# Kernel tuning notes

Measured on AMD Instinct MI355X. Metric: run time of the kernel, lower is better.

The kernel has to match this reference:

```python
import jax, jax.numpy as jnp
import numpy as np

B = 256; L = 512; PRED = 96; DVARS = 21
P = 16; STRIDE = 16
N = (L - P) // STRIDE + 1      # 32 patches
DM = P * P                     # d_model = 256
K = 5                          # DctAtt low-freq coeffs
EPS_BN = 1e-5


def _dct_mats(n_len):
    # torch_dct DCT-II / DCT-III as dense matrices (exact same scaling as torch_dct)
    n = jnp.arange(n_len, dtype=jnp.float32)
    C = jnp.cos(jnp.pi * (2.0 * n[None, :] + 1.0) * n[:, None] / (2.0 * n_len))  # (k, m)
    D2 = 2.0 * C                                  # dct(x, norm=None):  X = x @ D2.T
    w0 = jnp.where(n == 0, 0.5, 1.0)
    D3 = (C.T * w0[None, :]) / n_len              # idct(X, norm=None): x = X @ D3.T
    rL = jnp.sqrt(jnp.asarray(n_len, jnp.float32))
    s_ortho = jnp.where(n == 0, 0.5 / rL, 0.5 * jnp.sqrt(2.0) / rL)  # unnorm -> ortho scale
    return D2, D3, s_ortho


def _bn(x, g, b):
    # BatchNorm1d, training-mode batch stats (biased var), x: (B, C, Lc)
    m = jnp.mean(x, axis=(0, 2), keepdims=True)
    v = jnp.var(x, axis=(0, 2), keepdims=True)
    return g[None, :, None] * (x - m) * jax.lax.rsqrt(v + EPS_BN) + b[None, :, None]


def _gelu(x):
    return jax.nn.gelu(x, approximate=False)  # torch nn.GELU default = exact erf


def setup_inputs():
    key = jax.random.key(0)
    ks = jax.random.split(key, 24)
    r = lambda i, shp, s=0.02: jax.random.normal(ks[i], shp, jnp.float32) * s
    return dict(
        x=jax.random.normal(ks[0], (B, L, DVARS), jnp.float32),
        w_dct=r(1, (DVARS,), 0.2), b_dct=r(2, (DVARS,), 0.02),
        W_embed=r(3, (P, DM), 0.05), b_embed=r(4, (DM,), 0.02),
        W_linres=r(5, (N * DM, PRED), 0.01), b_linres=r(6, (PRED,), 0.02),
        W_dres=r(7, (DM, P), 0.05), b_dres=r(8, (P,), 0.02),
        w_dc=r(9, (N, P), 0.1), b_dc=r(10, (N,), 0.02),
        w_dc1=r(11, (N, 3), 0.2), b_dc1=r(12, (N,), 0.02),
        g_dctnorm=jnp.ones((DVARS,), jnp.float32), b_dctnorm=jnp.zeros((DVARS,), jnp.float32),
        g_patchnorm=jnp.ones((N,), jnp.float32), b_patchnorm=jnp.zeros((N,), jnp.float32),
        g_depthnorm=jnp.ones((N,), jnp.float32), b_depthnorm=jnp.zeros((N,), jnp.float32),
        thr_p=jnp.array([0.3], jnp.float32),
        W_m1=r(13, (L, PRED), 0.02), b_m1=r(14, (PRED,), 0.02),
        W_m2=r(15, (PRED, PRED), 0.05), b_m2=r(16, (PRED,), 0.02),
        a_dw_w=r(17, (K,), 0.2), a_dw_b=r(18, (), 0.02),
        a_cw=jnp.float32(1.0) + r(19, (), 0.1), a_cb=r(20, (), 0.02),
        a_g=jnp.ones((), jnp.float32), a_b=jnp.zeros((), jnp.float32),
    )


def reference(x, w_dct, b_dct, W_embed, b_embed, W_linres, b_linres,
              W_dres, b_dres, w_dc, b_dc, w_dc1, b_dc1,
              g_dctnorm, b_dctnorm, g_patchnorm, b_patchnorm,
              g_depthnorm, b_depthnorm, thr_p,
              W_m1, b_m1, W_m2, b_m2,
              a_dw_w, a_dw_b, a_cw, a_cb, a_g, a_b):
    Bx = x.shape[0]
    D2, D3, s_ortho = _dct_mats(L)
    xT = jnp.transpose(x, (0, 2, 1))                       # (B,D,L)
    # dctConv = depthwise 1x1 conv => per-channel scale+bias (same layer reused twice)
    x_res = xT * w_dct[:, None] + b_dct[:, None]
    z_dct = xT @ D2.T                                      # dct(norm=None)
    # adaptive_high_freq_mask
    energy = jnp.sum(z_dct * z_dct, axis=-1)               # (B,D)
    med = jnp.median(energy, axis=1, keepdims=True)
    norm_e = energy / (med + 1e-6)
    thr = jnp.quantile(norm_e, thr_p[0])                   # global quantile over all elems
    mask = (norm_e > thr).astype(x.dtype)[..., None]       # broadcasts over freq axis
    z = (z_dct * mask) * w_dct[:, None] + b_dct[:, None]
    z = _gelu(z)
    z = _bn(z, g_dctnorm, b_dctnorm)
    z1 = z @ D3.T + x_res                                  # idct + residual, (B,D,L)
    # patchify (unfold)
    idx = jnp.arange(N)[:, None] * STRIDE + jnp.arange(P)[None, :]
    zp = xT[..., idx].reshape(Bx * DVARS, N, P)            # (BD,N,P)
    z_p = zp @ W_embed + b_embed                           # (BD,N,DM)
    z_res = jnp.transpose(z_p.reshape(Bx, DVARS, N * DM) @ W_linres + b_linres, (0, 2, 1))
    res = z_p @ W_dres + b_dres                            # (BD,N,P)
    # depth_conv: depthwise conv, kernel=P, stride=P over DM=P*P
    zd = jnp.einsum('bnqp,np->bnq', z_p.reshape(Bx * DVARS, N, P, P), w_dc) + b_dc[:, None]
    zd = _bn(zd + res, g_patchnorm, b_patchnorm)
    z2 = _gelu(zd)
    # depth_conv1: depthwise k=3 pad=1
    zpad = jnp.pad(z2, ((0, 0), (0, 0), (1, 1)))
    zc = (w_dc1[:, 0, None] * zpad[..., :-2] + w_dc1[:, 1, None] * zpad[..., 1:-1]
          + w_dc1[:, 2, None] * zpad[..., 2:]) + b_dc1[:, None]
    zc = _bn(zc, g_depthnorm, b_depthnorm)
    zc = _gelu(zc) + z2
    z2f = zc.reshape(Bx, DVARS, N * P)                     # (B,D,L)
    # DctAtt on z1*z2f (low-freq pick + dwConv(k=5,stride=5) + BN(1) + GELU + 1x1 + softmax)
    prod = z1 * z2f
    low = (prod @ D2.T[:, :K]) * s_ortho[:K]               # ortho DCT, first K coeffs (B,D,K)
    att = low @ a_dw_w + a_dw_b                            # (B,D)
    m = jnp.mean(att); v = jnp.var(att)
    att = a_g * (att - m) * jax.lax.rsqrt(v + EPS_BN) + a_b
    att = _gelu(att)
    att1 = jax.nn.softmax(att * a_cw + a_cb, axis=-1)[..., None]  # (B,D,1)
    zsum = z1 * att1 + z2f * (1.0 - att1)
    z_mlp = _gelu(zsum @ W_m1 + b_m1) @ W_m2 + b_m2        # Mlp, (B,D,PRED)
    return z_res + jnp.transpose(z_mlp, (0, 2, 1))         # (B,PRED,D)
```

## Files before the change

kernel.cpp:

```cpp
#include <hip/hip_runtime.h>
#include <hip/hip_bf16.h>

#define B_    256
#define L_    512
#define DV    21
#define NROW  5376
#define NP    32
#define PP    16
#define PRED_ 96

static const size_t OFF_XT    = 0;
static const size_t OFF_ZA    = 2752512;
static const size_t OFF_Z1    = 5505024;
static const size_t OFF_ZCP   = 8257536;
static const size_t OFF_D2    = 11010048;
static const size_t OFF_D3    = 11272192;
static const size_t OFF_TN    = 11583488;
static const size_t OFF_TB    = 11591680;
static const size_t OFF_C     = 11592192;
static const size_t OFF_EN    = 11592320;
static const size_t OFF_NORM  = 11597696;
static const size_t OFF_ATT   = 11603072;
static const size_t OFF_ATT1  = 11608448;
static const size_t OFF_STAT  = 11613824;
static const size_t OFF_ABP   = 11614144;
static const size_t OFF_ABDEP = 11614208;
static const size_t OFF_FLAG  = 11614272;
static const size_t OFF_STG   = 11614336;
static const size_t OFF_T     = 12468816;
static const size_t OFF_PARTP = 15221328;
static const size_t OFF_PARTD = 15307344;
static const size_t OFF_EPART = 15393360;
static const size_t OFF_PARTM = 15436368;
static const size_t OFF_BCAT  = 15447120;
static const size_t OFF_PM    = 15512656;
static const size_t OFF_PC    = 15905872;

static const int S_WDCT=0, S_BDCT=24, S_WE=48, S_BE=4144, S_WL=4400, S_BL=790832,
  S_WD=790928, S_BDRES=795024, S_WDC=795040, S_BDC=795552, S_WDC1=795584, S_BDC1=795680,
  S_GD=795712, S_BDN=795736, S_GP=795760, S_BP=795792, S_GDEP=795824, S_BDEP=795856,
  S_THR=795888, S_WM1=795892, S_BM1=845044, S_WM2=845140, S_BM2=854356,
  S_ADWW=854452, S_ADWB=854460, S_ACW=854464, S_ACB=854468, S_AG=854472, S_AB2=854476;

struct Ptrs { const void* p[30]; };

typedef __attribute__((ext_vector_type(8))) short bf16x8;
typedef __attribute__((ext_vector_type(4))) short bf16x4;
typedef __attribute__((ext_vector_type(4))) float f32x4;

__device__ __forceinline__ float bf2f(unsigned short h){
  unsigned u = ((unsigned)h) << 16;
  return __uint_as_float(u);
}
__device__ __forceinline__ short f2b(float f){
  unsigned u = __float_as_uint(f);
  u = (u + 0x7FFFu + ((u >> 16) & 1u)) >> 16;
  return (short)u;
}
__device__ __forceinline__ float gelu_f(float x){ return 0.5f*x*(1.0f+erff(x*0.70710678118654752440f)); }

#define RD(P,I) (mode ? ((const float*)(P))[(I)] : bf2f(((const unsigned short*)(P))[(I)]))

__global__ __launch_bounds__(256) void k_setup(Ptrs ptrs, float* __restrict__ W,
    float* __restrict__ xt, unsigned short* __restrict__ D2h, unsigned short* __restrict__ D2l,
    unsigned short* __restrict__ D3h, float* __restrict__ dvec,
    float* __restrict__ PM, float* __restrict__ PC,
    float* __restrict__ Tn, float* __restrict__ tb){
  int b = blockIdx.x, tid = threadIdx.x;
  int mode = (((const unsigned*)ptrs.p[13])[0] == 0x3F800000u) ? 1 : 0;
  float* S = W + OFF_STG;
  if (b < 3338){
    const int cnt[29] = {21,21,4096,256,786432,96,4096,16,512,32,96,32,21,21,32,32,32,32,1,49152,96,9216,96,5,1,1,1,1,1};
    const int off[29] = {S_WDCT,S_BDCT,S_WE,S_BE,S_WL,S_BL,S_WD,S_BDRES,S_WDC,S_BDC,S_WDC1,S_BDC1,
                         S_GD,S_BDN,S_GP,S_BP,S_GDEP,S_BDEP,S_THR,S_WM1,S_BM1,S_WM2,S_BM2,
                         S_ADWW,S_ADWB,S_ACW,S_ACB,S_AG,S_AB2};
    int gid = b*256 + tid;
    int a = -1, loc = 0, base = 0;
    #pragma unroll
    for (int i = 0; i < 29; i++){
      if (a < 0 && gid < base + cnt[i]){ a = i; loc = gid - base; }
      base += cnt[i];
    }
    if (a < 0) return;
    S[off[a] + loc] = RD(ptrs.p[a+1], loc);
  } else if (b < 4362){
    __shared__ float xs[128*DV];
    int b2 = b - 3338;
    int bb = b2 >> 2, ch = b2 & 3;
    int l0 = ch*128;
    size_t base = (size_t)bb*(L_*DV) + (size_t)l0*DV;
    for (int i = tid; i < 128*DV; i += 256) xs[i] = RD(ptrs.p[0], base + i);
    __syncthreads();
    for (int i = tid; i < 128*DV; i += 256){
      int d = i >> 7, l = i & 127;
      xt[((size_t)bb*DV + d)*512 + l0 + l] = xs[l*DV + d];
    }
  } else if (b < 5386){
    int i = (b - 4362)*256 + tid;
    int kk = i >> 9, m = i & 511;
    const float PIo = 3.14159265358979323846f / 1024.0f;
    int a = ((2*m+1)*kk) & 2047;
    float v = 2.0f * cosf(PIo * (float)a);
    short hi = f2b(v);
    D2h[i] = (unsigned short)hi;
    D2l[i] = (unsigned short)f2b(v - bf2f((unsigned short)hi));
    int a2 = ((2*kk+1)*m) & 2047;
    float w0 = (m==0) ? 0.5f : 1.0f;
    D3h[i] = (unsigned short)f2b(cosf(PIo * (float)a2) * w0 * (1.0f/512.0f));
    if (i < 512){
      const float rs = 22.627416997969522f;
      float s = 0.f;
      #pragma unroll
      for (int k5 = 0; k5 < 5; k5++){
        float awk = RD(ptrs.p[24], k5);
        float sk = ((k5 == 0) ? 0.5f : 0.70710678118654752440f) / rs;
        int a5 = ((2*i+1)*k5) & 2047;
        s += 2.0f * cosf(PIo * (float)a5) * sk * awk;
      }
      dvec[i] = s;
    }
  } else if (b == 5386){
    W[OFF_STAT + tid] = 0.0f;
    if (tid == 0) *(int*)(W + OFF_FLAG) = mode;
  } else if (b < 6923){
    int bb2 = b - 5387;
    int y = bb2 / 192, xb = bb2 - y*192;
    int gid = xb*256 + tid;
    int l = gid/96, p = gid - l*96;
    int n = l>>4, q = l&15;
    int j0 = y*32;
    float acc = 0.f;
    #pragma unroll 8
    for (int j = j0; j < j0+32; j++)
      acc += RD(ptrs.p[3], q*256+j) * RD(ptrs.p[5], (size_t)(n*256+j)*96 + p);
    PM[(size_t)y*49152 + gid] = acc;
  } else if (b < 7051){
    int blkC = b - 6923;
    int rp = tid >> 7, p = tid & 127;
    if (p >= 96) return;
    float acc = 0.f;
    int J0 = blkC*64;
    for (int j = 0; j < 64; j += 2){
      int J = J0 + j + rp;
      acc += RD(ptrs.p[4], J & 255) * RD(ptrs.p[5], (size_t)J*96 + p);
    }
    if (blkC == 0 && rp == 0) acc += RD(ptrs.p[6], p);
    PC[(blkC*2 + rp)*96 + p] = acc;
  } else {
    __shared__ float WeS[4096];
    __shared__ float WdS[4096];
    __shared__ float wdcS[16];
    __shared__ float beS[256];
    __shared__ float bdresS[16];
    int n = b - 7051;
    for (int i = tid; i < 4096; i += 256){ WeS[i] = RD(ptrs.p[3], i); WdS[i] = RD(ptrs.p[7], i); }
    beS[tid] = RD(ptrs.p[4], tid);
    if (tid < 16){ wdcS[tid] = RD(ptrs.p[9], n*16 + tid); bdresS[tid] = RD(ptrs.p[8], tid); }
    __syncthreads();
    int q2 = tid>>4, q = tid&15;
    float R = 0.f;
    for (int j = 0; j < 256; j++) R += WeS[q2*256+j] * WdS[j*16+q];
    float G = 0.f;
    #pragma unroll
    for (int p = 0; p < 16; p++) G += WeS[q2*256 + q*16 + p] * wdcS[p];
    Tn[n*256 + q2*16 + q] = R + G;
    if (tid < 16){
      float rb = bdresS[tid];
      for (int j = 0; j < 256; j++) rb += beS[j] * WdS[j*16+tid];
      float gb = RD(ptrs.p[10], n);
      #pragma unroll
      for (int p = 0; p < 16; p++) gb += beS[tid*16+p] * wdcS[p];
      tb[n*16+tid] = rb + gb;
    }
  }
}

__global__ __launch_bounds__(256) void k_mega(
    const float* __restrict__ xt, const unsigned short* __restrict__ Bh16,
    const unsigned short* __restrict__ Bl16, float* __restrict__ C,
    float* __restrict__ e_part, const int* __restrict__ flag,
    const float* __restrict__ Tn, const float* __restrict__ tb,
    float* __restrict__ t, float* __restrict__ partP,
    const float* __restrict__ S, const float* __restrict__ PM,
    const float* __restrict__ PC, float* __restrict__ cb, unsigned short* __restrict__ Bt){
  int b = blockIdx.x, tid = threadIdx.x;
  if (b < 672){
    __shared__ short Ahi[64*40];
    __shared__ short Alo[64*40];
    __shared__ short Bhi[64*40];
    __shared__ short Blo[64*40];
    int mode = *flag;
    int bx = b & 7, by = b >> 3;
    int rowBase = by*64, colBase = bx*64;
    int srow = tid>>2, seg = tid&3;
    int r = rowBase + srow;
    int wave = tid>>6, lane = tid&63;
    int m = lane&15, quad = lane>>4;
    f32x4 acc[4] = {};
    for (int k0 = 0; k0 < 512; k0 += 32){
      float4 a0 = *(const float4*)(xt + (size_t)r*512 + k0 + seg*8);
      float4 a1 = *(const float4*)(xt + (size_t)r*512 + k0 + seg*8 + 4);
      bf16x8 ah;
      float av[8] = {a0.x,a0.y,a0.z,a0.w,a1.x,a1.y,a1.z,a1.w};
      #pragma unroll
      for (int j = 0; j < 8; j++) ah[j] = f2b(av[j]);
      *(bf16x8*)(Ahi + srow*40 + seg*8) = ah;
      if (mode){
        bf16x8 al;
        #pragma unroll
        for (int j = 0; j < 8; j++) al[j] = f2b(av[j] - bf2f((unsigned short)ah[j]));
        *(bf16x8*)(Alo + srow*40 + seg*8) = al;
      }
      *(bf16x8*)(Bhi + srow*40 + seg*8) = *(const bf16x8*)(Bh16 + (size_t)(colBase+srow)*512 + k0 + seg*8);
      *(bf16x8*)(Blo + srow*40 + seg*8) = *(const bf16x8*)(Bl16 + (size_t)(colBase+srow)*512 + k0 + seg*8);
      __syncthreads();
      bf16x8 afh = *(bf16x8*)(Ahi + (wave*16 + m)*40 + quad*8);
      #pragma unroll
      for (int tt = 0; tt < 4; tt++){
        bf16x8 bfh = *(bf16x8*)(Bhi + (tt*16 + m)*40 + quad*8);
        bf16x8 bfl = *(bf16x8*)(Blo + (tt*16 + m)*40 + quad*8);
        acc[tt] = __builtin_amdgcn_mfma_f32_16x16x32_bf16(afh, bfh, acc[tt], 0, 0, 0);
        acc[tt] = __builtin_amdgcn_mfma_f32_16x16x32_bf16(afh, bfl, acc[tt], 0, 0, 0);
      }
      if (mode){
        bf16x8 afl = *(bf16x8*)(Alo + (wave*16 + m)*40 + quad*8);
        #pragma unroll
        for (int tt = 0; tt < 4; tt++){
          bf16x8 bfh = *(bf16x8*)(Bhi + (tt*16 + m)*40 + quad*8);
          bf16x8 bfl = *(bf16x8*)(Blo + (tt*16 + m)*40 + quad*8);
          acc[tt] = __builtin_amdgcn_mfma_f32_16x16x32_bf16(afl, bfh, acc[tt], 0, 0, 0);
          acc[tt] = __builtin_amdgcn_mfma_f32_16x16x32_bf16(afl, bfl, acc[tt], 0, 0, 0);
        }
      }
      __syncthreads();
    }
    float es[4] = {};
    #pragma unroll
    for (int tt = 0; tt < 4; tt++){
      #pragma unroll
      for (int i = 0; i < 4; i++){
        int rr = rowBase + wave*16 + quad*4 + i;
        int cc = colBase + tt*16 + m;
        float v = acc[tt][i];
        C[(size_t)rr*512 + cc] = v;
        es[i] += v*v;
      }
    }
    #pragma unroll
    for (int off = 1; off < 16; off <<= 1){
      #pragma unroll
      for (int i = 0; i < 4; i++) es[i] += __shfl_xor(es[i], off);
    }
    if (m == 0){
      #pragma unroll
      for (int i = 0; i < 4; i++){
        int rr = rowBase + wave*16 + quad*4 + i;
        e_part[rr*8 + bx] = es[i];
      }
    }
  } else if (b < 2016){
    int blk = b - 672;
    int n0 = tid >> 4, qq = tid & 15;
    int n1 = n0 + 16;
    float T0[16], T1[16];
    #pragma unroll
    for (int q2 = 0; q2 < 16; q2++){
      T0[q2] = Tn[n0*256 + q2*16 + qq];
      T1[q2] = Tn[n1*256 + q2*16 + qq];
    }
    float tb0 = tb[n0*16 + qq], tb1 = tb[n1*16 + qq];
    float s0 = 0.f, q0 = 0.f, s1 = 0.f, q1 = 0.f;
    #pragma unroll
    for (int rr = 0; rr < 4; rr++){
      int r = blk*4 + rr;
      float x0 = xt[(size_t)r*512 + tid];
      float x1 = xt[(size_t)r*512 + tid + 256];
      float a0 = tb0, a1 = tb1;
      #pragma unroll
      for (int q2 = 0; q2 < 16; q2++){
        a0 += __shfl(x0, q2, 16) * T0[q2];
        a1 += __shfl(x1, q2, 16) * T1[q2];
      }
      t[(size_t)r*512 + tid] = a0;       s0 += a0; q0 += a0*a0;
      t[(size_t)r*512 + tid + 256] = a1; s1 += a1; q1 += a1*a1;
    }
    #pragma unroll
    for (int off = 1; off < 16; off <<= 1){
      s0 += __shfl_xor(s0, off); q0 += __shfl_xor(q0, off);
      s1 += __shfl_xor(s1, off); q1 += __shfl_xor(q1, off);
    }
    if (qq == 0){
      partP[(2*n0)*1344 + blk] = s0; partP[(2*n0+1)*1344 + blk] = q0;
      partP[(2*n1)*1344 + blk] = s1; partP[(2*n1+1)*1344 + blk] = q1;
    }
  } else if (b < 2528){
    int i = (b - 2016)*256 + tid;
    int cc = i >> 9, mm = i & 511;
    float v = 0.f;
    if (cc < 96) v = S[S_WM1 + mm*96 + cc];
    else if (cc >= 128 && cc < 224){
      int idx = mm*96 + (cc - 128);
      #pragma unroll
      for (int y = 0; y < 8; y++) v += PM[(size_t)y*49152 + idx];
    }
    Bt[i] = (unsigned short)f2b(v);
  } else {
    if (tid < 96){
      float a = 0.f;
      for (int j = 0; j < 256; j++) a += PC[j*96 + tid];
      cb[tid] = a;
    }
  }
}

__device__ __forceinline__ void dev_bnfin(const float* part, int P, const float* g,
    const float* bb, float count, float* ab, int c, int tid){
  const float* ps = part + (size_t)(2*c)*P;
  const float* pq = part + (size_t)(2*c+1)*P;
  float s = 0.f, s2 = 0.f;
  for (int i = tid; i < P; i += 256){ s += ps[i]; s2 += pq[i]; }
  for (int off = 32; off; off >>= 1){ s += __shfl_down(s, off); s2 += __shfl_down(s2, off); }
  __shared__ float ws[4][2];
  if ((tid & 63) == 0){ ws[tid>>6][0] = s; ws[tid>>6][1] = s2; }
  __syncthreads();
  if (tid == 0){
    float S1 = ws[0][0]+ws[1][0]+ws[2][0]+ws[3][0];
    float S2 = ws[0][1]+ws[1][1]+ws[2][1]+ws[3][1];
    float mean = S1 / count;
    float var  = S2 / count - mean*mean;
    float al = g[c] * rsqrtf(var + 1e-5f);
    float be = bb[c] - mean * al;
    ab[2*c] = al; ab[2*c+1] = be;
  }
}

__global__ __launch_bounds__(256) void k_mid1(const float* __restrict__ e_part,
    float* __restrict__ en, float* __restrict__ norm,
    const float* __restrict__ partP, const float* __restrict__ S, float* __restrict__ abp){
  int b = blockIdx.x, tid = threadIdx.x;
  if (b == 0){
    for (int r = tid; r < NROW; r += 256){
      float s = 0.f;
      #pragma unroll
      for (int j = 0; j < 8; j++) s += e_part[r*8 + j];
      en[r] = s;
    }
    __syncthreads();
    int bb = tid;
    float v[DV];
    for (int d = 0; d < DV; d++) v[d] = en[bb*DV + d];
    float med = 0.f;
    for (int i = 0; i < DV; i++){
      int rk = 0;
      for (int j = 0; j < DV; j++) rk += (v[j] < v[i]) || (v[j] == v[i] && j < i);
      if (rk == 10) med = v[i];
    }
    float den = med + 1e-6f;
    for (int d = 0; d < DV; d++) norm[bb*DV + d] = v[d] / den;
  } else {
    dev_bnfin(partP, 1344, S + S_GP, S + S_BP, 86016.0f, abp, b - 1, tid);
  }
}

__global__ __launch_bounds__(256) void k_mid2(const float* __restrict__ norm,
    const float* __restrict__ S, float* __restrict__ stat,
    float* __restrict__ t, float* __restrict__ zcp,
    const float* __restrict__ abp, float* __restrict__ partD){
  int b = blockIdx.x, tid = threadIdx.x;
  if (b < 336){
    int cand = tid >> 4, part = tid & 15;
    int idx = b*16 + cand;
    float val = norm[idx];
    int cnt = 0;
    int j0 = part*336;
    for (int j = j0; j < j0 + 336; ++j){
      float v = norm[j];
      cnt += (v < val) || (v == val && j < idx);
    }
    __shared__ int sc[16][17];
    sc[cand][part] = cnt;
    __syncthreads();
    if (part == 0){
      int rank = 0;
      #pragma unroll
      for (int i = 0; i < 16; i++) rank += sc[cand][i];
      float q = S[S_THR];
      float pos = q * 5375.0f;
      int i0 = (int)floorf(pos);
      int i1 = (i0 + 1 > 5375) ? 5375 : i0 + 1;
      if (rank == i0) stat[200] = val;
      if (rank == i1) stat[201] = val;
    }
  } else {
    int blk = b - 336;
    const float* wdc1 = S + S_WDC1;
    const float* bdc1 = S + S_BDC1;
    int n0 = tid >> 4, qq = tid & 15;
    int n1 = n0 + 16;
    float al0 = abp[2*n0], be0 = abp[2*n0+1], al1 = abp[2*n1], be1 = abp[2*n1+1];
    float w00 = wdc1[n0*3], w01 = wdc1[n0*3+1], w02 = wdc1[n0*3+2], bb0 = bdc1[n0];
    float w10 = wdc1[n1*3], w11 = wdc1[n1*3+1], w12 = wdc1[n1*3+2], bb1 = bdc1[n1];
    float s0 = 0.f, q0 = 0.f, s1 = 0.f, q1 = 0.f;
    #pragma unroll
    for (int rr = 0; rr < 4; rr++){
      int r = blk*4 + rr;
      float v0 = t[(size_t)r*512 + tid];
      float v1 = t[(size_t)r*512 + tid + 256];
      float z0  = gelu_f(al0*v0 + be0);
      float z1v = gelu_f(al1*v1 + be1);
      float l0 = __shfl_up(z0, 1, 16);    if (qq == 0)  l0 = 0.f;
      float r0 = __shfl_down(z0, 1, 16);  if (qq == 15) r0 = 0.f;
      float l1 = __shfl_up(z1v, 1, 16);   if (qq == 0)  l1 = 0.f;
      float r1 = __shfl_down(z1v, 1, 16); if (qq == 15) r1 = 0.f;
      float cv0 = w00*l0 + w01*z0  + w02*r0 + bb0;
      float cv1 = w10*l1 + w11*z1v + w12*r1 + bb1;
      zcp[(size_t)r*512 + tid] = cv0;       t[(size_t)r*512 + tid] = z0;
      zcp[(size_t)r*512 + tid + 256] = cv1; t[(size_t)r*512 + tid + 256] = z1v;
      s0 += cv0; q0 += cv0*cv0; s1 += cv1; q1 += cv1*cv1;
    }
    #pragma unroll
    for (int off = 1; off < 16; off <<= 1){
      s0 += __shfl_xor(s0, off); q0 += __shfl_xor(q0, off);
      s1 += __shfl_xor(s1, off); q1 += __shfl_xor(q1, off);
    }
    if (qq == 0){
      partD[(2*n0)*1344 + blk] = s0; partD[(2*n0+1)*1344 + blk] = q0;
      partD[(2*n1)*1344 + blk] = s1; partD[(2*n1+1)*1344 + blk] = q1;
    }
  }
}

__global__ __launch_bounds__(256) void k_mid3(float* __restrict__ zA, const float* __restrict__ norm,
    const float* __restrict__ stat, const float* __restrict__ S,
    float* __restrict__ partM, const float* __restrict__ partD, float* __restrict__ abdep){
  int b = blockIdx.x, tid = threadIdx.x;
  if (b < NROW){
    int r = b;
    int d = r % DV, brow = r / DV;
    float q = S[S_THR];
    float pos = q * 5375.0f; float f = pos - floorf(pos);
    float thr = stat[200] + (stat[201] - stat[200]) * f;
    float mask = norm[r] > thr ? 1.0f : 0.0f;
    float w = S[S_WDCT + d], bb = S[S_BDCT + d];
    float s = 0.f, s2 = 0.f;
    for (int i = tid; i < 512; i += 256){
      float v = zA[(size_t)r*512 + i] * mask * w + bb;
      float g = gelu_f(v);
      zA[(size_t)r*512 + i] = g;
      s += g; s2 += g*g;
    }
    for (int off = 32; off; off >>= 1){ s += __shfl_down(s, off); s2 += __shfl_down(s2, off); }
    __shared__ float wsum[4][2];
    int wv = tid >> 6;
    if ((tid & 63) == 0){ wsum[wv][0] = s; wsum[wv][1] = s2; }
    __syncthreads();
    if (tid == 0){
      float SS  = wsum[0][0]+wsum[1][0]+wsum[2][0]+wsum[3][0];
      float SS2 = wsum[0][1]+wsum[1][1]+wsum[2][1]+wsum[3][1];
      partM[(2*d)*256 + brow] = SS;
      partM[(2*d+1)*256 + brow] = SS2;
    }
  } else {
    dev_bnfin(partD, 1344, S + S_GDEP, S + S_BDEP, 86016.0f, abdep, b - NROW, tid);
  }
}

__global__ __launch_bounds__(256) void k_gemm1(
    const float* __restrict__ A, const unsigned short* __restrict__ Bg,
    float* __restrict__ C, const float* __restrict__ partM, const float* __restrict__ xt,
    const float* __restrict__ S){
  __shared__ short Ah[64*40];
  __shared__ short Bh[64*40];
  __shared__ float redS[84];
  __shared__ float abdS[42];
  int tid = threadIdx.x;
  if (tid < 84){
    int s = tid >> 1, h = tid & 1;
    const float* ps = partM + (size_t)s*256 + h*128;
    float a = 0.f;
    #pragma unroll 16
    for (int i = 0; i < 128; i++) a += ps[i];
    redS[tid] = a;
  }
  __syncthreads();
  if (tid < DV){
    float S1 = redS[(2*tid)*2] + redS[(2*tid)*2+1];
    float S2 = redS[(2*tid+1)*2] + redS[(2*tid+1)*2+1];
    float mean = S1 / 131072.0f;
    float var  = S2 / 131072.0f - mean*mean;
    float al = S[S_GD + tid] * rsqrtf(var + 1e-5f);
    abdS[2*tid] = al;
    abdS[2*tid+1] = S[S_BDN + tid] - mean * al;
  }
  __syncthreads();
  int rowBase = blockIdx.y*64, colBase = blockIdx.x*64;
  int srow = tid>>2, seg = tid&3;
  int r = rowBase + srow;
  int d0 = r % DV;
  float alpha = abdS[2*d0], beta = abdS[2*d0+1];
  int wave = tid>>6, lane = tid&63;
  int m = lane&15, quad = lane>>4;
  f32x4 acc[4] = {};
  for (int k0 = 0; k0 < 512; k0 += 32){
    float4 a0 = *(const float4*)(A + (size_t)r*512 + k0 + seg*8);
    float4 a1 = *(const float4*)(A + (size_t)r*512 + k0 + seg*8 + 4);
    a0.x = alpha*a0.x+beta; a0.y = alpha*a0.y+beta; a0.z = alpha*a0.z+beta; a0.w = alpha*a0.w+beta;
    a1.x = alpha*a1.x+beta; a1.y = alpha*a1.y+beta; a1.z = alpha*a1.z+beta; a1.w = alpha*a1.w+beta;
    bf16x8 av;
    av[0]=f2b(a0.x); av[1]=f2b(a0.y); av[2]=f2b(a0.z); av[3]=f2b(a0.w);
    av[4]=f2b(a1.x); av[5]=f2b(a1.y); av[6]=f2b(a1.z); av[7]=f2b(a1.w);
    *(bf16x8*)(Ah + srow*40 + seg*8) = av;
    bf16x8 bv = *(const bf16x8*)(Bg + (size_t)(colBase+srow)*512 + k0 + seg*8);
    *(bf16x8*)(Bh + srow*40 + seg*8) = bv;
    __syncthreads();
    bf16x8 af = *(bf16x8*)(Ah + (wave*16 + m)*40 + quad*8);
    #pragma unroll
    for (int t = 0; t < 4; t++){
      bf16x8 bf = *(bf16x8*)(Bh + (t*16 + m)*40 + quad*8);
      acc[t] = __builtin_amdgcn_mfma_f32_16x16x32_bf16(af, bf, acc[t], 0, 0, 0);
    }
    __syncthreads();
  }
  #pragma unroll
  for (int t = 0; t < 4; t++){
    #pragma unroll
    for (int i = 0; i < 4; i++){
      int rr = rowBase + wave*16 + quad*4 + i;
      int cc = colBase + t*16 + m;
      int d = rr % DV;
      float v = acc[t][i] + xt[(size_t)rr*512 + cc]*S[S_WDCT + d] + S[S_BDCT + d];
      C[(size_t)rr*512 + cc] = v;
    }
  }
}

__global__ __launch_bounds__(256) void k_z2fatt(float* __restrict__ zcp, const float* __restrict__ z2,
    const float* __restrict__ ab, const float* __restrict__ z1,
    const float* __restrict__ dvec, float* __restrict__ att){
  int r = blockIdx.x, tid = threadIdx.x;
  size_t base = (size_t)r*512;
  float s = 0.f;
  #pragma unroll
  for (int h = 0; h < 2; h++){
    int idx = tid + h*256;
    int n = (idx >> 4) & 31;
    float v = gelu_f(ab[2*n]*zcp[base+idx] + ab[2*n+1]) + z2[base+idx];
    zcp[base+idx] = v;
    s += z1[base+idx] * v * dvec[idx];
  }
  for (int off = 32; off; off >>= 1) s += __shfl_down(s, off);
  __shared__ float ws[4];
  if ((tid & 63) == 0) ws[tid>>6] = s;
  __syncthreads();
  if (tid == 0) att[r] = ws[0]+ws[1]+ws[2]+ws[3];
}

__global__ __launch_bounds__(256) void k_gemm_out(
    const float* __restrict__ z1, const float* __restrict__ zcp, const float* __restrict__ xt,
    const unsigned short* __restrict__ Bg, const float* __restrict__ att,
    const float* __restrict__ cb, const float* __restrict__ S,
    void* __restrict__ outv, const int* __restrict__ flag){
  __shared__ short Amix[16*40];
  __shared__ short Axt[16*40];
  __shared__ short Bst[256*40];
  __shared__ float Hs[16*260];
  __shared__ float att1S[16];
  __shared__ float asum[2];
  __shared__ float ws[4][2];
  int bb = blockIdx.x, tid = threadIdx.x;
  int r0 = bb*16;
  {
    float s = 0.f, s2 = 0.f;
    for (int i = tid; i < NROW; i += 256){ float a = att[i]; s += a; s2 += a*a; }
    for (int off = 32; off; off >>= 1){ s += __shfl_down(s, off); s2 += __shfl_down(s2, off); }
    if ((tid & 63) == 0){ ws[tid>>6][0] = s; ws[tid>>6][1] = s2; }
    __syncthreads();
    if (tid == 0){
      asum[0] = ws[0][0]+ws[1][0]+ws[2][0]+ws[3][0];
      asum[1] = ws[0][1]+ws[1][1]+ws[2][1]+ws[3][1];
    }
    __syncthreads();
  }
  if (tid < 16){
    int r = r0 + tid; int b2 = r / DV, d = r - b2*DV;
    float mean = asum[0] / 5376.0f;
    float var  = asum[1] / 5376.0f - mean*mean;
    float al = S[S_AG] * rsqrtf(var + 1e-5f);
    float bbx = S[S_AB2];
    float cw = S[S_ACW], cb2 = S[S_ACB];
    float v[DV]; float mx = -1e30f;
    for (int dd = 0; dd < DV; dd++){
      float a = att[b2*DV + dd];
      a = gelu_f(al*(a - mean) + bbx);
      a = a*cw + cb2;
      v[dd] = a; mx = fmaxf(mx, a);
    }
    float ss = 0.f;
    for (int dd = 0; dd < DV; dd++) ss += expf(v[dd] - mx);
    att1S[tid] = expf(v[d] - mx) / ss;
  }
  __syncthreads();
  int wave = tid>>6, lane = tid&63;
  int m = lane&15, quad = lane>>4;
  f32x4 acc[4] = {};
  for (int k0 = 0; k0 < 512; k0 += 32){
    if (tid < 128){
      int srow = tid >> 3, seg = tid & 7;
      int r = r0 + srow;
      float a1r = att1S[srow];
      float4 zf = *(const float4*)(z1  + (size_t)r*512 + k0 + seg*4);
      float4 cf = *(const float4*)(zcp + (size_t)r*512 + k0 + seg*4);
      float om = 1.0f - a1r;
      bf16x4 mv;
      mv[0] = f2b(a1r*zf.x + om*cf.x); mv[1] = f2b(a1r*zf.y + om*cf.y);
      mv[2] = f2b(a1r*zf.z + om*cf.z); mv[3] = f2b(a1r*zf.w + om*cf.w);
      *(bf16x4*)(Amix + srow*40 + seg*4) = mv;
      float4 xf = *(const float4*)(xt + (size_t)r*512 + k0 + seg*4);
      bf16x4 xv;
      xv[0] = f2b(xf.x); xv[1] = f2b(xf.y); xv[2] = f2b(xf.z); xv[3] = f2b(xf.w);
      *(bf16x4*)(Axt + srow*40 + seg*4) = xv;
    }
    #pragma unroll
    for (int cg = 0; cg < 4; cg++){
      int col = cg*64 + (tid>>2);
      *(bf16x8*)(Bst + col*40 + (tid&3)*8) = *(const bf16x8*)(Bg + (size_t)col*512 + k0 + (tid&3)*8);
    }
    __syncthreads();
    const short* Ast = (wave < 2) ? Amix : Axt;
    bf16x8 af = *(bf16x8*)(Ast + m*40 + quad*8);
    #pragma unroll
    for (int tc = 0; tc < 4; tc++){
      bf16x8 bf = *(bf16x8*)(Bst + (wave*64 + tc*16 + m)*40 + quad*8);
      acc[tc] = __builtin_amdgcn_mfma_f32_16x16x32_bf16(af, bf, acc[tc], 0, 0, 0);
    }
    __syncthreads();
  }
  #pragma unroll
  for (int tc = 0; tc < 4; tc++){
    #pragma unroll
    for (int i = 0; i < 4; i++){
      int col = wave*64 + tc*16 + m;
      Hs[(quad*4 + i)*260 + col] = acc[tc][i];
    }
  }
  __syncthreads();
  for (int i = tid; i < 16*96; i += 256){
    int rr = i / 96, k = i - rr*96;
    Hs[rr*260 + k] = gelu_f(Hs[rr*260 + k] + S[S_BM1 + k]);
  }
  __syncthreads();
  int rr = tid >> 4, pg = tid & 15;
  const float* W2g = S + S_WM2;
  float accv[6] = {};
  for (int k = 0; k < 96; k++){
    float h = Hs[rr*260 + k];
    #pragma unroll
    for (int j = 0; j < 6; j++) accv[j] += h * W2g[k*96 + pg*6 + j];
  }
  int rg = r0 + rr;
  int b2 = rg / DV, d = rg - b2*DV;
  int mode = *flag;
  #pragma unroll
  for (int j = 0; j < 6; j++){
    int p = pg*6 + j;
    float val = Hs[rr*260 + 128 + p] + cb[p] + accv[j] + S[S_BM2 + p];
    size_t oi = ((size_t)b2*96 + p)*DV + d;
    if (mode) ((float*)outv)[oi] = val;
    else ((__hip_bfloat16*)outv)[oi] = __float2bfloat16(val);
  }
}

extern "C" void kernel_launch(void* const* d_in, const int* in_sizes, int n_in,
                              void* d_out, int out_size, void* d_ws, size_t ws_size,
                              hipStream_t stream) {
  float* w = (float*)d_ws;
  float* xt   = w + OFF_XT;
  float* zA   = w + OFF_ZA;
  float* z1   = w + OFF_Z1;
  float* zcp  = w + OFF_ZCP;
  unsigned short* D2h = (unsigned short*)(w + OFF_D2);
  unsigned short* D2l = (unsigned short*)(w + OFF_D2 + 131072);
  unsigned short* D3h = (unsigned short*)(w + OFF_D3);
  float* Tn   = w + OFF_TN;
  float* tb   = w + OFF_TB;
  float* cb   = w + OFF_C;
  float* en   = w + OFF_EN;
  float* nrm  = w + OFF_NORM;
  float* att  = w + OFF_ATT;
  float* dvec = w + OFF_ATT1;
  float* stat = w + OFF_STAT;
  float* abp  = w + OFF_ABP;
  float* abdep= w + OFF_ABDEP;
  int*   flag = (int*)(w + OFF_FLAG);
  float* S    = w + OFF_STG;
  float* tbuf = w + OFF_T;
  float* partP = w + OFF_PARTP;
  float* partD = w + OFF_PARTD;
  float* e_part= w + OFF_EPART;
  float* partM = w + OFF_PARTM;
  unsigned short* BcatTh = (unsigned short*)(w + OFF_BCAT);
  float* PM   = w + OFF_PM;
  float* PC   = w + OFF_PC;

  Ptrs ptrs;
  for (int i = 0; i < 30; i++) ptrs.p[i] = d_in[i];

  k_setup<<<7083, 256, 0, stream>>>(ptrs, w, xt, D2h, D2l, D3h, dvec, PM, PC, Tn, tb);
  k_mega<<<2529, 256, 0, stream>>>(xt, D2h, D2l, zA, e_part, flag, Tn, tb, tbuf, partP, S, PM, PC, cb, BcatTh);
  k_mid1<<<33, 256, 0, stream>>>(e_part, en, nrm, partP, S, abp);
  k_mid2<<<1680, 256, 0, stream>>>(nrm, S, stat, tbuf, zcp, abp, partD);
  k_mid3<<<NROW + NP, 256, 0, stream>>>(zA, nrm, stat, S, partM, partD, abdep);
  k_gemm1<<<dim3(8,84), 256, 0, stream>>>(zA, D3h, z1, partM, xt, S);
  k_z2fatt<<<NROW, 256, 0, stream>>>(zcp, tbuf, abdep, z1, dvec, att);
  k_gemm_out<<<336, 256, 0, stream>>>(z1, zcp, xt, BcatTh, att, cb, S, d_out, flag);
}
```

Before: 291.0 us.

## Store intermediate activation buffers in bf16 instead of fp32

Converts the intermediate tensors (zA, z1, zcp, t) that flow between kernels from fp32 to bf16 storage, halving their global memory read and write traffic. Each of the five downstream kernels now converts on load and store. The values were already rounded to bf16 before the MFMA GEMMs, but elementwise paths such as the gelu and residual sums, the attention dot products and the stats inputs now see bf16-rounded data. This adds precision risk against the fp32 reference.

```diff
diff --git a/kernel.cpp b/kernel.cpp
--- a/kernel.cpp
+++ b/kernel.cpp
@@ -177,10 +177,10 @@
 
 __global__ __launch_bounds__(256) void k_mega(
     const float* __restrict__ xt, const unsigned short* __restrict__ Bh16,
-    const unsigned short* __restrict__ Bl16, float* __restrict__ C,
+    const unsigned short* __restrict__ Bl16, unsigned short* __restrict__ Ch,
     float* __restrict__ e_part, const int* __restrict__ flag,
     const float* __restrict__ Tn, const float* __restrict__ tb,
-    float* __restrict__ t, float* __restrict__ partP,
+    unsigned short* __restrict__ th, float* __restrict__ partP,
     const float* __restrict__ S, const float* __restrict__ PM,
     const float* __restrict__ PC, float* __restrict__ cb, unsigned short* __restrict__ Bt){
   int b = blockIdx.x, tid = threadIdx.x;
@@ -242,7 +242,7 @@
         int rr = rowBase + wave*16 + quad*4 + i;
         int cc = colBase + tt*16 + m;
         float v = acc[tt][i];
-        C[(size_t)rr*512 + cc] = v;
+        Ch[(size_t)rr*512 + cc] = (unsigned short)f2b(v);
         es[i] += v*v;
       }
     }
@@ -281,8 +281,8 @@
         a0 += __shfl(x0, q2, 16) * T0[q2];
         a1 += __shfl(x1, q2, 16) * T1[q2];
       }
-      t[(size_t)r*512 + tid] = a0;       s0 += a0; q0 += a0*a0;
-      t[(size_t)r*512 + tid + 256] = a1; s1 += a1; q1 += a1*a1;
+      th[(size_t)r*512 + tid] = (unsigned short)f2b(a0);       s0 += a0; q0 += a0*a0;
+      th[(size_t)r*512 + tid + 256] = (unsigned short)f2b(a1); s1 += a1; q1 += a1*a1;
     }
     #pragma unroll
     for (int off = 1; off < 16; off <<= 1){
@@ -364,7 +364,7 @@
 
 __global__ __launch_bounds__(256) void k_mid2(const float* __restrict__ norm,
     const float* __restrict__ S, float* __restrict__ stat,
-    float* __restrict__ t, float* __restrict__ zcp,
+    unsigned short* __restrict__ th, unsigned short* __restrict__ zch,
     const float* __restrict__ abp, float* __restrict__ partD){
   int b = blockIdx.x, tid = threadIdx.x;
   if (b < 336){
@@ -404,8 +404,8 @@
     #pragma unroll
     for (int rr = 0; rr < 4; rr++){
       int r = blk*4 + rr;
-      float v0 = t[(size_t)r*512 + tid];
-      float v1 = t[(size_t)r*512 + tid + 256];
+      float v0 = bf2f(th[(size_t)r*512 + tid]);
+      float v1 = bf2f(th[(size_t)r*512 + tid + 256]);
       float z0  = gelu_f(al0*v0 + be0);
       float z1v = gelu_f(al1*v1 + be1);
       float l0 = __shfl_up(z0, 1, 16);    if (qq == 0)  l0 = 0.f;
@@ -414,8 +414,10 @@
       float r1 = __shfl_down(z1v, 1, 16); if (qq == 15) r1 = 0.f;
       float cv0 = w00*l0 + w01*z0  + w02*r0 + bb0;
       float cv1 = w10*l1 + w11*z1v + w12*r1 + bb1;
-      zcp[(size_t)r*512 + tid] = cv0;       t[(size_t)r*512 + tid] = z0;
-      zcp[(size_t)r*512 + tid + 256] = cv1; t[(size_t)r*512 + tid + 256] = z1v;
+      zch[(size_t)r*512 + tid] = (unsigned short)f2b(cv0);
+      th[(size_t)r*512 + tid]  = (unsigned short)f2b(z0);
+      zch[(size_t)r*512 + tid + 256] = (unsigned short)f2b(cv1);
+      th[(size_t)r*512 + tid + 256]  = (unsigned short)f2b(z1v);
       s0 += cv0; q0 += cv0*cv0; s1 += cv1; q1 += cv1*cv1;
     }
     #pragma unroll
@@ -430,7 +432,7 @@
   }
 }
 
-__global__ __launch_bounds__(256) void k_mid3(float* __restrict__ zA, const float* __restrict__ norm,
+__global__ __launch_bounds__(256) void k_mid3(unsigned short* __restrict__ zAh, const float* __restrict__ norm,
     const float* __restrict__ stat, const float* __restrict__ S,
     float* __restrict__ partM, const float* __restrict__ partD, float* __restrict__ abdep){
   int b = blockIdx.x, tid = threadIdx.x;
@@ -444,9 +446,9 @@
     float w = S[S_WDCT + d], bb = S[S_BDCT + d];
     float s = 0.f, s2 = 0.f;
     for (int i = tid; i < 512; i += 256){
-      float v = zA[(size_t)r*512 + i] * mask * w + bb;
+      float v = bf2f(zAh[(size_t)r*512 + i]) * mask * w + bb;
       float g = gelu_f(v);
-      zA[(size_t)r*512 + i] = g;
+      zAh[(size_t)r*512 + i] = (unsigned short)f2b(g);
       s += g; s2 += g*g;
     }
     for (int off = 32; off; off >>= 1){ s += __shfl_down(s, off); s2 += __shfl_down(s2, off); }
@@ -466,8 +468,8 @@
 }
 
 __global__ __launch_bounds__(256) void k_gemm1(
-    const float* __restrict__ A, const unsigned short* __restrict__ Bg,
-    float* __restrict__ C, const float* __restrict__ partM, const float* __restrict__ xt,
+    const unsigned short* __restrict__ Ah16, const unsigned short* __restrict__ Bg,
+    unsigned short* __restrict__ Ch, const float* __restrict__ partM, const float* __restrict__ xt,
     const float* __restrict__ S){
   __shared__ short Ah[64*40];
   __shared__ short Bh[64*40];
@@ -502,13 +504,10 @@
   int m = lane&15, quad = lane>>4;
   f32x4 acc[4] = {};
   for (int k0 = 0; k0 < 512; k0 += 32){
-    float4 a0 = *(const float4*)(A + (size_t)r*512 + k0 + seg*8);
-    float4 a1 = *(const float4*)(A + (size_t)r*512 + k0 + seg*8 + 4);
-    a0.x = alpha*a0.x+beta; a0.y = alpha*a0.y+beta; a0.z = alpha*a0.z+beta; a0.w = alpha*a0.w+beta;
-    a1.x = alpha*a1.x+beta; a1.y = alpha*a1.y+beta; a1.z = alpha*a1.z+beta; a1.w = alpha*a1.w+beta;
+    bf16x8 ar = *(const bf16x8*)((const short*)Ah16 + (size_t)r*512 + k0 + seg*8);
     bf16x8 av;
-    av[0]=f2b(a0.x); av[1]=f2b(a0.y); av[2]=f2b(a0.z); av[3]=f2b(a0.w);
-    av[4]=f2b(a1.x); av[5]=f2b(a1.y); av[6]=f2b(a1.z); av[7]=f2b(a1.w);
+    #pragma unroll
+    for (int j = 0; j < 8; j++) av[j] = f2b(alpha*bf2f((unsigned short)ar[j]) + beta);
     *(bf16x8*)(Ah + srow*40 + seg*8) = av;
     bf16x8 bv = *(const bf16x8*)(Bg + (size_t)(colBase+srow)*512 + k0 + seg*8);
     *(bf16x8*)(Bh + srow*40 + seg*8) = bv;
@@ -529,14 +528,15 @@
       int cc = colBase + t*16 + m;
       int d = rr % DV;
       float v = acc[t][i] + xt[(size_t)rr*512 + cc]*S[S_WDCT + d] + S[S_BDCT + d];
-      C[(size_t)rr*512 + cc] = v;
-    }
-  }
-}
-
-__global__ __launch_bounds__(256) void k_z2fatt(float* __restrict__ zcp, const float* __restrict__ z2,
-    const float* __restrict__ ab, const float* __restrict__ z1,
-    const float* __restrict__ dvec, float* __restrict__ att){
+      Ch[(size_t)rr*512 + cc] = (unsigned short)f2b(v);
+    }
+  }
+}
+
+__global__ __launch_bounds__(256) void k_z2fatt(unsigned short* __restrict__ zch,
+    const unsigned short* __restrict__ th, const float* __restrict__ ab,
+    const unsigned short* __restrict__ z1h, const float* __restrict__ dvec,
+    float* __restrict__ att){
   int r = blockIdx.x, tid = threadIdx.x;
   size_t base = (size_t)r*512;
   float s = 0.f;
@@ -544,9 +544,9 @@
   for (int h = 0; h < 2; h++){
     int idx = tid + h*256;
     int n = (idx >> 4) & 31;
-    float v = gelu_f(ab[2*n]*zcp[base+idx] + ab[2*n+1]) + z2[base+idx];
-    zcp[base+idx] = v;
-    s += z1[base+idx] * v * dvec[idx];
+    float v = gelu_f(ab[2*n]*bf2f(zch[base+idx]) + ab[2*n+1]) + bf2f(th[base+idx]);
+    zch[base+idx] = (unsigned short)f2b(v);
+    s += bf2f(z1h[base+idx]) * v * dvec[idx];
   }
   for (int off = 32; off; off >>= 1) s += __shfl_down(s, off);
   __shared__ float ws[4];
@@ -556,7 +556,8 @@
 }
 
 __global__ __launch_bounds__(256) void k_gemm_out(
-    const float* __restrict__ z1, const float* __restrict__ zcp, const float* __restrict__ xt,
+    const unsigned short* __restrict__ z1h, const unsigned short* __restrict__ zch,
+    const float* __restrict__ xt,
     const unsigned short* __restrict__ Bg, const float* __restrict__ att,
     const float* __restrict__ cb, const float* __restrict__ S,
     void* __restrict__ outv, const int* __restrict__ flag){
@@ -608,12 +609,13 @@
       int srow = tid >> 3, seg = tid & 7;
       int r = r0 + srow;
       float a1r = att1S[srow];
-      float4 zf = *(const float4*)(z1  + (size_t)r*512 + k0 + seg*4);
-      float4 cf = *(const float4*)(zcp + (size_t)r*512 + k0 + seg*4);
       float om = 1.0f - a1r;
+      bf16x4 zf = *(const bf16x4*)((const short*)z1h + (size_t)r*512 + k0 + seg*4);
+      bf16x4 cf = *(const bf16x4*)((const short*)zch + (size_t)r*512 + k0 + seg*4);
       bf16x4 mv;
-      mv[0] = f2b(a1r*zf.x + om*cf.x); mv[1] = f2b(a1r*zf.y + om*cf.y);
-      mv[2] = f2b(a1r*zf.z + om*cf.z); mv[3] = f2b(a1r*zf.w + om*cf.w);
+      #pragma unroll
+      for (int j = 0; j < 4; j++)
+        mv[j] = f2b(a1r*bf2f((unsigned short)zf[j]) + om*bf2f((unsigned short)cf[j]));
       *(bf16x4*)(Amix + srow*40 + seg*4) = mv;
       float4 xf = *(const float4*)(xt + (size_t)r*512 + k0 + seg*4);
       bf16x4 xv;
@@ -675,9 +677,9 @@
                               hipStream_t stream) {
   float* w = (float*)d_ws;
   float* xt   = w + OFF_XT;
-  float* zA   = w + OFF_ZA;
-  float* z1   = w + OFF_Z1;
-  float* zcp  = w + OFF_ZCP;
+  unsigned short* zAh = (unsigned short*)(w + OFF_ZA);
+  unsigned short* z1h = (unsigned short*)(w + OFF_Z1);
+  unsigned short* zch = (unsigned short*)(w + OFF_ZCP);
   unsigned short* D2h = (unsigned short*)(w + OFF_D2);
   unsigned short* D2l = (unsigned short*)(w + OFF_D2 + 131072);
   unsigned short* D3h = (unsigned short*)(w + OFF_D3);
@@ -693,7 +695,7 @@
   float* abdep= w + OFF_ABDEP;
   int*   flag = (int*)(w + OFF_FLAG);
   float* S    = w + OFF_STG;
-  float* tbuf = w + OFF_T;
+  unsigned short* th = (unsigned short*)(w + OFF_T);
   float* partP = w + OFF_PARTP;
   float* partD = w + OFF_PARTD;
   float* e_part= w + OFF_EPART;
@@ -706,11 +708,11 @@
   for (int i = 0; i < 30; i++) ptrs.p[i] = d_in[i];
 
   k_setup<<<7083, 256, 0, stream>>>(ptrs, w, xt, D2h, D2l, D3h, dvec, PM, PC, Tn, tb);
-  k_mega<<<2529, 256, 0, stream>>>(xt, D2h, D2l, zA, e_part, flag, Tn, tb, tbuf, partP, S, PM, PC, cb, BcatTh);
+  k_mega<<<2529, 256, 0, stream>>>(xt, D2h, D2l, zAh, e_part, flag, Tn, tb, th, partP, S, PM, PC, cb, BcatTh);
   k_mid1<<<33, 256, 0, stream>>>(e_part, en, nrm, partP, S, abp);
-  k_mid2<<<1680, 256, 0, stream>>>(nrm, S, stat, tbuf, zcp, abp, partD);
-  k_mid3<<<NROW + NP, 256, 0, stream>>>(zA, nrm, stat, S, partM, partD, abdep);
-  k_gemm1<<<dim3(8,84), 256, 0, stream>>>(zA, D3h, z1, partM, xt, S);
-  k_z2fatt<<<NROW, 256, 0, stream>>>(zcp, tbuf, abdep, z1, dvec, att);
-  k_gemm_out<<<336, 256, 0, stream>>>(z1, zcp, xt, BcatTh, att, cb, S, d_out, flag);
-}
+  k_mid2<<<1680, 256, 0, stream>>>(nrm, S, stat, th, zch, abp, partD);
+  k_mid3<<<NROW + NP, 256, 0, stream>>>(zAh, nrm, stat, S, partM, partD, abdep);
+  k_gemm1<<<dim3(8,84), 256, 0, stream>>>(zAh, D3h, z1h, partM, xt, S);
+  k_z2fatt<<<NROW, 256, 0, stream>>>(zch, th, abdep, z1h, dvec, att);
+  k_gemm_out<<<336, 256, 0, stream>>>(z1h, zch, xt, BcatTh, att, cb, S, d_out, flag);
+}
```

New measurement: 281.8 us. -3.2%, faster.
